# Optimization experiments

Hardware: AMD Instinct MI355X
Metric: run time of the kernel (lower is better)

## Reference

```python
import jax, jax.numpy as jnp
import numpy as np

B, C, IMG, P = 8, 3, 384, 16
D, H, L, MLP, NCLS = 384, 6, 12, 1536, 1000
G = IMG // P
T = G * G + 1  # 577 tokens incl CLS
GAMMA, MIN_TOKENS, EPS = 0.1, 16, 1e-6
LN_EPS = 1e-5


def _ln(x, s, b):
    m = x.mean(-1, keepdims=True)
    v = ((x - m) ** 2).mean(-1, keepdims=True)
    return (x - m) / jnp.sqrt(v + LN_EPS) * s + b


def _attn_block(xn, qw, qb, pw, pb):
    Bt, Tt, Dd = xn.shape
    hd = Dd // H
    qkv = (xn @ qw + qb).reshape(Bt, Tt, 3, H, hd).transpose(2, 0, 3, 1, 4)
    q, k, v = qkv[0], qkv[1], qkv[2]
    attn = jax.nn.softmax(jnp.einsum('bhqd,bhkd->bhqk', q, k) * (hd ** -0.5), axis=-1)
    out = jnp.einsum('bhqk,bhkd->bhqd', attn, v).transpose(0, 2, 1, 3).reshape(Bt, Tt, Dd)
    return attn, v, out @ pw + pb


def _cls_sensitivity(attn):
    # normalized entropy of the CLS attention row, mean over heads -> [B]
    cls = attn[:, :, 0, :]
    ent = -(cls * jnp.log(cls + EPS)).sum(-1)
    return (ent / jnp.log(float(attn.shape[-1]))).mean(1)


def _jacobian_importance(attn, v):
    # d(CLS)/d(patch_j) approx: CLS attention to patch j weighted by ||v_j||, summed over heads
    vnorm = jnp.linalg.norm(v, axis=-1)                   # [B,H,T]
    raw = (attn[:, :, 0, 1:] * vnorm[:, :, 1:]).sum(1)    # [B,N]
    mass = raw.sum(-1)                                    # [B]
    return raw / (mass[:, None] + EPS), mass


def _keep_ratio(rho, mass, prev_mass):
    delta = jnp.abs(mass - prev_mass) / (prev_mass + EPS)
    return jnp.clip(1.0 - GAMMA * (rho.mean() + delta.mean()), 0.0, 1.0)


def _mlp(xm, w1, b1, w2, b2):
    return jax.nn.gelu(xm @ w1 + b1, approximate=False) @ w2 + b2


def setup_inputs():
    key = jax.random.key(0)
    ks = jax.random.split(key, 9)
    s = 0.02
    return {
        'x': jax.random.normal(ks[0], (B, C, IMG, IMG), jnp.float32),
        'patch_w': jax.random.normal(ks[1], (C * P * P, D), jnp.float32) * s,
        'patch_b': jnp.zeros((D,), jnp.float32),
        'cls_token': jax.random.normal(ks[2], (1, 1, D), jnp.float32) * s,
        'pos_embed': jax.random.normal(ks[3], (1, T, D), jnp.float32) * s,
        'ln1_s': jnp.ones((L, D), jnp.float32), 'ln1_b': jnp.zeros((L, D), jnp.float32),
        'qkv_w': jax.random.normal(ks[4], (L, D, 3 * D), jnp.float32) * s,
        'qkv_b': jnp.zeros((L, 3 * D), jnp.float32),
        'proj_w': jax.random.normal(ks[5], (L, D, D), jnp.float32) * s,
        'proj_b': jnp.zeros((L, D), jnp.float32),
        'ln2_s': jnp.ones((L, D), jnp.float32), 'ln2_b': jnp.zeros((L, D), jnp.float32),
        'fc1_w': jax.random.normal(ks[6], (L, D, MLP), jnp.float32) * s,
        'fc1_b': jnp.zeros((L, MLP), jnp.float32),
        'fc2_w': jax.random.normal(ks[7], (L, MLP, D), jnp.float32) * s,
        'fc2_b': jnp.zeros((L, D), jnp.float32),
        'norm_s': jnp.ones((D,), jnp.float32), 'norm_b': jnp.zeros((D,), jnp.float32),
        'head_w': jax.random.normal(ks[8], (D, NCLS), jnp.float32) * s,
        'head_b': jnp.zeros((NCLS,), jnp.float32),
    }


def reference(x, patch_w, patch_b, cls_token, pos_embed, ln1_s, ln1_b, qkv_w, qkv_b,
              proj_w, proj_b, ln2_s, ln2_b, fc1_w, fc1_b, fc2_w, fc2_b,
              norm_s, norm_b, head_w, head_b):
    # NOTE: runs eagerly (no jit) because per-layer token counts are data-dependent,
    # mirroring the torch module's CPU syncs for index selection.
    Bc = x.shape[0]
    # patch embed: stride==kernel conv as a reshape+GEMM
    patches = x.reshape(Bc, C, G, P, G, P).transpose(0, 2, 4, 1, 3, 5).reshape(Bc, G * G, C * P * P)
    tok = patches @ patch_w + patch_b
    xcur = jnp.concatenate([jnp.broadcast_to(cls_token, (Bc, 1, D)), tok], axis=1) + pos_embed
    N = xcur.shape[1] - 1
    prev_mass = None
    for l in range(L):
        xn = _ln(xcur, ln1_s[l], ln1_b[l])
        attn, v, ao = _attn_block(xn, qkv_w[l], qkv_b[l], proj_w[l], proj_b[l])
        xcur = xcur + ao
        xcur = xcur + _mlp(_ln(xcur, ln2_s[l], ln2_b[l]), fc1_w[l], fc1_b[l], fc2_w[l], fc2_b[l])
        if N <= MIN_TOKENS:
            continue
        rho = _cls_sensitivity(attn)
        importance, mass = _jacobian_importance(attn, v)
        if prev_mass is not None:
            kr = float(_keep_ratio(rho, mass, prev_mass))
            N_next = max(MIN_TOKENS, int(N * kr))
        else:
            N_next = N
        if N_next < N:
            scores = importance.mean(0)  # shared across batch, matches x[:, keep_idx]
            _, idx = jax.lax.top_k(scores, N_next)
            keep = jnp.concatenate([jnp.zeros((1,), idx.dtype), jnp.sort(idx) + 1])
            xcur = xcur[:, keep]
            N = N_next
        prev_mass = mass
    xf = _ln(xcur, norm_s, norm_b)
    return xf[:, 0] @ head_w + head_b
```

## Files before the change

### kernel.cpp

```cpp
#include <hip/hip_runtime.h>
#include <math.h>

#define NHEADS 6
#define DMODEL 384
#define TMAXT  577
#define NMAXT  576
#define BATCH  8
#define LAYERS 12

typedef __attribute__((ext_vector_type(8))) short bf16x8v;
typedef __attribute__((ext_vector_type(4))) float f32x4v;

#define XSZ      (8ull*577*384)
#define X0_OFF   0ull
#define X1_OFF   (X0_OFF + XSZ)
#define XN_OFF   (X1_OFF + XSZ)
#define QKV_OFF  (XN_OFF + XSZ)
#define QKV_SZ   (8ull*577*1152)
#define AO_OFF   (QKV_OFF + QKV_SZ)
#define HBELEM   (8ull*577*1536)
#define RAWH_OFF (AO_OFF + XSZ)
#define RAWH_SZ  (8ull*6*576)
#define ENT_OFF  (RAWH_OFF + RAWH_SZ)
#define PM_OFF   (ENT_OFF + 64)
#define XF_OFF   (PM_OFF + 64)
#define KEEP_OFF (XF_OFF + 8*384)
#define T_OFF    (KEEP_OFF + 640)
#define TN_OFF   (T_OFF + 16)
#define WSPL_OFF (TN_OFF + 16)

#define W_QKV   0ull
#define W_PROJ  884736ull
#define W_FC1   1179648ull
#define W_FC2   2359296ull
#define W_PATCH 3538944ull

__device__ inline unsigned short rne_bf16(float f) {
    unsigned int u = __float_as_uint(f);
    u += 0x7FFFu + ((u >> 16) & 1u);
    return (unsigned short)(u >> 16);
}
__device__ inline float bf16_to_f(unsigned short h) {
    return __uint_as_float(((unsigned int)h) << 16);
}
__device__ inline void split_bf16(float x, unsigned short& h, unsigned short& l) {
    h = rne_bf16(x);
    l = rne_bf16(x - bf16_to_f(h));
}

__global__ __launch_bounds__(128) void prologue_kernel(const float* __restrict__ cls_tok,
                                                       const float* __restrict__ pos,
                                                       float* __restrict__ x0,
                                                       int* __restrict__ dT0)
{
    int b = blockIdx.x;
    for (int d = threadIdx.x; d < 384; d += 128)
        x0[(size_t)b*577*384 + d] = cls_tok[d] + pos[d];
    if (b == 0 && threadIdx.x == 0) *dT0 = 577;
}

__global__ __launch_bounds__(256) void psplit_kernel(const float* __restrict__ W,
                                                     unsigned short* __restrict__ dst,
                                                     int K, int N)
{
    int ktiles = K >> 5, ntiles = N >> 5;
    int tid = blockIdx.x;
    if (tid >= ktiles * ntiles) return;
    int tk = tid % ktiles, tn = tid / ktiles;
    int k0 = tk << 5, n0 = tn << 5;
    __shared__ unsigned short Th[32][34];
    __shared__ unsigned short Tl[32][34];
    int t = threadIdx.x;
    {
        int row = t >> 3, c4 = (t & 7) << 2;
        float4 wv = *(const float4*)(W + (size_t)(k0 + row) * N + n0 + c4);
        unsigned short h, l;
        split_bf16(wv.x, h, l); Th[c4+0][row] = h; Tl[c4+0][row] = l;
        split_bf16(wv.y, h, l); Th[c4+1][row] = h; Tl[c4+1][row] = l;
        split_bf16(wv.z, h, l); Th[c4+2][row] = h; Tl[c4+2][row] = l;
        split_bf16(wv.w, h, l); Th[c4+3][row] = h; Tl[c4+3][row] = l;
    }
    __syncthreads();
    {
        int n = t >> 3, k4 = (t & 7) << 2;
        unsigned short* dh = dst + (size_t)(n0 + n) * K + k0 + k4;
        unsigned short* dl = dh + (size_t)K * N;
        *(ushort4*)dh = make_ushort4(Th[n][k4], Th[n][k4+1], Th[n][k4+2], Th[n][k4+3]);
        *(ushort4*)dl = make_ushort4(Tl[n][k4], Tl[n][k4+1], Tl[n][k4+2], Tl[n][k4+3]);
    }
}

__global__ __launch_bounds__(256) void wsplit_kernel(const float* __restrict__ qkvw,
                                                     const float* __restrict__ projw,
                                                     const float* __restrict__ fc1w,
                                                     const float* __restrict__ fc2w,
                                                     unsigned short* __restrict__ wspl)
{
    int mat = blockIdx.y;
    const float* W; int K, N; size_t off;
    if (mat == 0)      { W = qkvw; K = 384;  N = 1152; off = W_QKV; }
    else if (mat == 1) { W = projw; K = 384; N = 384;  off = W_PROJ; }
    else if (mat == 2) { W = fc1w; K = 384;  N = 1536; off = W_FC1; }
    else               { W = fc2w; K = 1536; N = 384;  off = W_FC2; }
    int ktiles = K >> 5, ntiles = N >> 5;
    int tid = blockIdx.x;
    if (tid >= ktiles * ntiles) return;
    int tk = tid % ktiles, tn = tid / ktiles;
    int k0 = tk << 5, n0 = tn << 5;
    __shared__ unsigned short Th[32][34];
    __shared__ unsigned short Tl[32][34];
    int t = threadIdx.x;
    {
        int row = t >> 3, c4 = (t & 7) << 2;
        float4 wv = *(const float4*)(W + (size_t)(k0 + row) * N + n0 + c4);
        unsigned short h, l;
        split_bf16(wv.x, h, l); Th[c4+0][row] = h; Tl[c4+0][row] = l;
        split_bf16(wv.y, h, l); Th[c4+1][row] = h; Tl[c4+1][row] = l;
        split_bf16(wv.z, h, l); Th[c4+2][row] = h; Tl[c4+2][row] = l;
        split_bf16(wv.w, h, l); Th[c4+3][row] = h; Tl[c4+3][row] = l;
    }
    __syncthreads();
    {
        int n = t >> 3, k4 = (t & 7) << 2;
        unsigned short* dh = wspl + off + (size_t)(n0 + n) * K + k0 + k4;
        unsigned short* dl = dh + (size_t)K * N;
        *(ushort4*)dh = make_ushort4(Th[n][k4], Th[n][k4+1], Th[n][k4+2], Th[n][k4+3]);
        *(ushort4*)dl = make_ushort4(Tl[n][k4], Tl[n][k4+1], Tl[n][k4+2], Tl[n][k4+3]);
    }
}

__global__ __launch_bounds__(256, 4) void patch_mfma_kernel(const float* __restrict__ x,
                                                            const unsigned short* __restrict__ Wt,
                                                            const float* __restrict__ pb,
                                                            const float* __restrict__ pos,
                                                            float* __restrict__ x0)
{
    const int K = 768, N = 384, M = 4608;
    int m0 = blockIdx.y * 64;
    int n0 = blockIdx.x * 64;

    __shared__ unsigned short As[2][64][40];
    __shared__ unsigned short Bs[2][64][40];

    int t = threadIdx.x;
    int lane = t & 63, w = t >> 6;
    int wr = w >> 1, wc = w & 1;
    int quad = lane >> 4, l16 = lane & 15;

    f32x4v acc[2][2];
#pragma unroll
    for (int i = 0; i < 2; i++)
#pragma unroll
        for (int j = 0; j < 2; j++) acc[i][j] = (f32x4v){0.f, 0.f, 0.f, 0.f};

    int arow = t >> 2, ak8 = (t & 3) * 8;
    int garow = m0 + arow;
    int ab = garow / 576, att = garow % 576;
    int g1 = att / 24, g2 = att % 24;
    const float* xr = x + ((size_t)(ab*3)*384 + g1*16)*384 + g2*16;

    int bn = t >> 2, bk8 = (t & 3) * 8;
    const unsigned short* Bh = Wt + (size_t)(n0 + bn) * K + bk8;
    const unsigned short* Bl = Bh + (size_t)K * N;

    for (int k0 = 0; k0 < K; k0 += 32) {
        int k = k0 + ak8;
        int c = k >> 8, rr = k & 255, p1 = rr >> 4, p2 = rr & 15;
        const float* src = xr + ((size_t)c*384 + p1)*384 + p2;
        float4 f0 = *(const float4*)(src);
        float4 f1 = *(const float4*)(src + 4);
        float f[8] = {f0.x, f0.y, f0.z, f0.w, f1.x, f1.y, f1.z, f1.w};
        unsigned short ah[8], al[8];
#pragma unroll
        for (int j = 0; j < 8; j++) split_bf16(f[j], ah[j], al[j]);
        uint4 vbh = *(const uint4*)(Bh + k0);
        uint4 vbl = *(const uint4*)(Bl + k0);
        __syncthreads();
        *(uint4*)&As[0][arow][ak8] = *(uint4*)ah;
        *(uint4*)&As[1][arow][ak8] = *(uint4*)al;
        *(uint4*)&Bs[0][bn][bk8] = vbh;
        *(uint4*)&Bs[1][bn][bk8] = vbl;
        __syncthreads();

        bf16x8v afh[2], afl[2], bfh[2], bfl[2];
#pragma unroll
        for (int rb = 0; rb < 2; rb++) {
            int r = wr * 32 + rb * 16 + l16;
            afh[rb] = *(const bf16x8v*)&As[0][r][quad * 8];
            afl[rb] = *(const bf16x8v*)&As[1][r][quad * 8];
        }
#pragma unroll
        for (int cb = 0; cb < 2; cb++) {
            int cc = wc * 32 + cb * 16 + l16;
            bfh[cb] = *(const bf16x8v*)&Bs[0][cc][quad * 8];
            bfl[cb] = *(const bf16x8v*)&Bs[1][cc][quad * 8];
        }
#pragma unroll
        for (int rb = 0; rb < 2; rb++)
#pragma unroll
            for (int cb = 0; cb < 2; cb++) {
                acc[rb][cb] = __builtin_amdgcn_mfma_f32_16x16x32_bf16(afl[rb], bfh[cb], acc[rb][cb], 0, 0, 0);
                acc[rb][cb] = __builtin_amdgcn_mfma_f32_16x16x32_bf16(afh[rb], bfl[cb], acc[rb][cb], 0, 0, 0);
                acc[rb][cb] = __builtin_amdgcn_mfma_f32_16x16x32_bf16(afh[rb], bfh[cb], acc[rb][cb], 0, 0, 0);
            }
    }

#pragma unroll
    for (int rb = 0; rb < 2; rb++) {
#pragma unroll
        for (int reg = 0; reg < 4; reg++) {
            int r = m0 + wr * 32 + rb * 16 + quad * 4 + reg;
            if (r >= M) continue;
            int bb = r / 576, ttt = r % 576;
#pragma unroll
            for (int cb = 0; cb < 2; cb++) {
                int cc = n0 + wc * 32 + cb * 16 + l16;
                float v = acc[rb][cb][reg] + pb[cc] + pos[(size_t)(1 + ttt)*384 + cc];
                x0[(size_t)(bb*577 + 1 + ttt)*384 + cc] = v;
            }
        }
    }
}

__global__ __launch_bounds__(256) void ln_kernel(const float* __restrict__ xin,
                                                 const float* __restrict__ sc,
                                                 const float* __restrict__ bi,
                                                 unsigned short* __restrict__ yhi,
                                                 unsigned short* __restrict__ ylo,
                                                 const int* __restrict__ dT)
{
    int T = *dT;
    int M = 8 * T;
    int r = blockIdx.x * 4 + (threadIdx.x >> 6);
    if (r >= M) return;
    int lane = threadIdx.x & 63;
    const float* xr = xin + (size_t)r * 384;
    float v[6];
#pragma unroll
    for (int i = 0; i < 6; i++) v[i] = xr[lane + 64*i];
    float s = v[0]+v[1]+v[2]+v[3]+v[4]+v[5];
#pragma unroll
    for (int off = 32; off; off >>= 1) s += __shfl_xor(s, off, 64);
    float mean = s * (1.0f/384.0f);
    float q = 0.f;
#pragma unroll
    for (int i = 0; i < 6; i++) { float d = v[i]-mean; q += d*d; }
#pragma unroll
    for (int off = 32; off; off >>= 1) q += __shfl_xor(q, off, 64);
    float rstd = 1.0f / sqrtf(q * (1.0f/384.0f) + 1e-5f);
#pragma unroll
    for (int i = 0; i < 6; i++) {
        int d = lane + 64*i;
        float y = (v[i]-mean) * rstd * sc[d] + bi[d];
        unsigned short h, l;
        split_bf16(y, h, l);
        yhi[(size_t)r*384 + d] = h;
        ylo[(size_t)r*384 + d] = l;
    }
}

template<bool GELU>
__global__ __launch_bounds__(256, 3) void gemm3_kernel(const unsigned short* __restrict__ Ahi,
                                                       const unsigned short* __restrict__ Alo,
                                                       const unsigned short* __restrict__ Wt,
                                                       const float* __restrict__ bias,
                                                       unsigned short* __restrict__ Chi,
                                                       unsigned short* __restrict__ Clo,
                                                       int K, int N,
                                                       const int* __restrict__ dT)
{
    int T = *dT; int M = 8 * T;
    int m0 = blockIdx.y * 64;
    if (m0 >= M) return;
    int n0 = blockIdx.x * 128;

    __shared__ unsigned short As[2][64][40];
    __shared__ unsigned short Bs[2][128][40];

    int t = threadIdx.x;
    int lane = t & 63, w = t >> 6;
    int wr = w >> 1, wc = w & 1;
    int quad = lane >> 4, l16 = lane & 15;

    f32x4v acc[2][4];
#pragma unroll
    for (int i = 0; i < 2; i++)
#pragma unroll
        for (int j = 0; j < 4; j++) acc[i][j] = (f32x4v){0.f, 0.f, 0.f, 0.f};

    int arow = t >> 2, ak = (t & 3) * 8;
    int ag = m0 + arow; if (ag > M - 1) ag = M - 1;
    const unsigned short* Ah = Ahi + (size_t)ag * K + ak;
    const unsigned short* Al = Alo + (size_t)ag * K + ak;

    int bn = t >> 1, bk = (t & 1) * 16;
    const unsigned short* Bh = Wt + (size_t)(n0 + bn) * K + bk;
    const unsigned short* Bl = Bh + (size_t)K * N;

    for (int k0 = 0; k0 < K; k0 += 32) {
        uint4 vah  = *(const uint4*)(Ah + k0);
        uint4 val  = *(const uint4*)(Al + k0);
        uint4 vbh0 = *(const uint4*)(Bh + k0);
        uint4 vbh1 = *(const uint4*)(Bh + k0 + 8);
        uint4 vbl0 = *(const uint4*)(Bl + k0);
        uint4 vbl1 = *(const uint4*)(Bl + k0 + 8);
        __syncthreads();
        *(uint4*)&As[0][arow][ak] = vah;
        *(uint4*)&As[1][arow][ak] = val;
        *(uint4*)&Bs[0][bn][bk]     = vbh0;
        *(uint4*)&Bs[0][bn][bk + 8] = vbh1;
        *(uint4*)&Bs[1][bn][bk]     = vbl0;
        *(uint4*)&Bs[1][bn][bk + 8] = vbl1;
        __syncthreads();

        bf16x8v afh[2], afl[2], bfh[4], bfl[4];
#pragma unroll
        for (int rb = 0; rb < 2; rb++) {
            int r = wr * 32 + rb * 16 + l16;
            afh[rb] = *(const bf16x8v*)&As[0][r][quad * 8];
            afl[rb] = *(const bf16x8v*)&As[1][r][quad * 8];
        }
#pragma unroll
        for (int cb = 0; cb < 4; cb++) {
            int c = wc * 64 + cb * 16 + l16;
            bfh[cb] = *(const bf16x8v*)&Bs[0][c][quad * 8];
            bfl[cb] = *(const bf16x8v*)&Bs[1][c][quad * 8];
        }
#pragma unroll
        for (int rb = 0; rb < 2; rb++)
#pragma unroll
            for (int cb = 0; cb < 4; cb++) {
                acc[rb][cb] = __builtin_amdgcn_mfma_f32_16x16x32_bf16(afl[rb], bfh[cb], acc[rb][cb], 0, 0, 0);
                acc[rb][cb] = __builtin_amdgcn_mfma_f32_16x16x32_bf16(afh[rb], bfl[cb], acc[rb][cb], 0, 0, 0);
                acc[rb][cb] = __builtin_amdgcn_mfma_f32_16x16x32_bf16(afh[rb], bfh[cb], acc[rb][cb], 0, 0, 0);
            }
    }

#pragma unroll
    for (int rb = 0; rb < 2; rb++) {
#pragma unroll
        for (int reg = 0; reg < 4; reg++) {
            int r = m0 + wr * 32 + rb * 16 + quad * 4 + reg;
            if (r >= M) continue;
#pragma unroll
            for (int cb = 0; cb < 4; cb++) {
                int c = n0 + wc * 64 + cb * 16 + l16;
                float v = acc[rb][cb][reg] + bias[c];
                if (GELU) v = 0.5f * v * (1.0f + erff(v * 0.70710678118654752440f));
                unsigned short h, l;
                split_bf16(v, h, l);
                Chi[(size_t)r * N + c] = h;
                Clo[(size_t)r * N + c] = l;
            }
        }
    }
}

__global__ __launch_bounds__(256, 4) void gemm64_kernel(const unsigned short* __restrict__ Ahi,
                                                        const unsigned short* __restrict__ Alo,
                                                        const unsigned short* __restrict__ Wt,
                                                        const float* __restrict__ bias,
                                                        const float* __restrict__ resid,
                                                        float* __restrict__ Cf,
                                                        int K, int N,
                                                        const int* __restrict__ dT)
{
    int T = *dT; int M = 8 * T;
    int m0 = blockIdx.y * 64;
    if (m0 >= M) return;
    int n0 = blockIdx.x * 64;

    __shared__ unsigned short As[2][64][40];
    __shared__ unsigned short Bs[2][64][40];

    int t = threadIdx.x;
    int lane = t & 63, w = t >> 6;
    int wr = w >> 1, wc = w & 1;
    int quad = lane >> 4, l16 = lane & 15;

    f32x4v acc[2][2];
#pragma unroll
    for (int i = 0; i < 2; i++)
#pragma unroll
        for (int j = 0; j < 2; j++) acc[i][j] = (f32x4v){0.f, 0.f, 0.f, 0.f};

    int arow = t >> 2, ak = (t & 3) * 8;
    int ag = m0 + arow; if (ag > M - 1) ag = M - 1;
    const unsigned short* Ah = Ahi + (size_t)ag * K + ak;
    const unsigned short* Al = Alo + (size_t)ag * K + ak;

    int bn = t >> 2, bk = (t & 3) * 8;
    const unsigned short* Bh = Wt + (size_t)(n0 + bn) * K + bk;
    const unsigned short* Bl = Bh + (size_t)K * N;

    for (int k0 = 0; k0 < K; k0 += 32) {
        uint4 vah = *(const uint4*)(Ah + k0);
        uint4 val = *(const uint4*)(Al + k0);
        uint4 vbh = *(const uint4*)(Bh + k0);
        uint4 vbl = *(const uint4*)(Bl + k0);
        __syncthreads();
        *(uint4*)&As[0][arow][ak] = vah;
        *(uint4*)&As[1][arow][ak] = val;
        *(uint4*)&Bs[0][bn][bk] = vbh;
        *(uint4*)&Bs[1][bn][bk] = vbl;
        __syncthreads();

        bf16x8v afh[2], afl[2], bfh[2], bfl[2];
#pragma unroll
        for (int rb = 0; rb < 2; rb++) {
            int r = wr * 32 + rb * 16 + l16;
            afh[rb] = *(const bf16x8v*)&As[0][r][quad * 8];
            afl[rb] = *(const bf16x8v*)&As[1][r][quad * 8];
        }
#pragma unroll
        for (int cb = 0; cb < 2; cb++) {
            int c = wc * 32 + cb * 16 + l16;
            bfh[cb] = *(const bf16x8v*)&Bs[0][c][quad * 8];
            bfl[cb] = *(const bf16x8v*)&Bs[1][c][quad * 8];
        }
#pragma unroll
        for (int rb = 0; rb < 2; rb++)
#pragma unroll
            for (int cb = 0; cb < 2; cb++) {
                acc[rb][cb] = __builtin_amdgcn_mfma_f32_16x16x32_bf16(afl[rb], bfh[cb], acc[rb][cb], 0, 0, 0);
                acc[rb][cb] = __builtin_amdgcn_mfma_f32_16x16x32_bf16(afh[rb], bfl[cb], acc[rb][cb], 0, 0, 0);
                acc[rb][cb] = __builtin_amdgcn_mfma_f32_16x16x32_bf16(afh[rb], bfh[cb], acc[rb][cb], 0, 0, 0);
            }
    }

#pragma unroll
    for (int rb = 0; rb < 2; rb++) {
#pragma unroll
        for (int reg = 0; reg < 4; reg++) {
            int r = m0 + wr * 32 + rb * 16 + quad * 4 + reg;
            if (r >= M) continue;
#pragma unroll
            for (int cb = 0; cb < 2; cb++) {
                int c = n0 + wc * 32 + cb * 16 + l16;
                float v = acc[rb][cb][reg] + bias[c] + resid[(size_t)r * N + c];
                Cf[(size_t)r * N + c] = v;
            }
        }
    }
}

__global__ __launch_bounds__(256, 3) void attn_kernel(const unsigned short* __restrict__ qh,
                                                      const unsigned short* __restrict__ ql,
                                                      unsigned short* __restrict__ out_hi,
                                                      unsigned short* __restrict__ out_lo,
                                                      const int* __restrict__ dT)
{
    int T = *dT;
    int q0 = blockIdx.x * 64;
    if (q0 >= T) return;
    int bh = blockIdx.y;
    int b = bh / NHEADS, h = bh % NHEADS;

    __shared__ unsigned short Ks[2][64][72];
    __shared__ unsigned short Vt[2][64][72];
    __shared__ float Ss[64][66];
    __shared__ float m_s[64], l_s[64], al_s[64];

    int t = threadIdx.x;
    int lane = t & 63, w = t >> 6;
    int l16 = lane & 15, quad = lane >> 4;

    const bf16x8v zf = (bf16x8v){0,0,0,0,0,0,0,0};
    bf16x8v qf[2][2];
    {
        int gq = q0 + w * 16 + l16;
        bool valid = gq < T;
        size_t base = (size_t)(b * T + (valid ? gq : 0)) * 1152 + h * 64;
#pragma unroll
        for (int ks = 0; ks < 2; ks++) {
            int off = ks * 32 + quad * 8;
            qf[ks][0] = valid ? *(const bf16x8v*)(qh + base + off) : zf;
            qf[ks][1] = valid ? *(const bf16x8v*)(ql + base + off) : zf;
        }
    }
    if (t < 64) { m_s[t] = -INFINITY; l_s[t] = 0.f; }

    f32x4v oacc[4];
#pragma unroll
    for (int cb = 0; cb < 4; cb++) oacc[cb] = (f32x4v){0.f, 0.f, 0.f, 0.f};

    int ntiles = (T + 63) >> 6;
    for (int kt = 0; kt < ntiles; kt++) {
        int kbase = kt * 64;
        __syncthreads();

        {
            int gk = kbase + lane;
            int sd0 = w * 16;
            bool valid = gk < T;
            size_t base = (size_t)(b * T + (valid ? gk : 0)) * 1152 + 384 + h * 64 + sd0;
            const uint4 z4 = make_uint4(0,0,0,0);
            uint4 kh0 = valid ? *(const uint4*)(qh + base)     : z4;
            uint4 kh1 = valid ? *(const uint4*)(qh + base + 8) : z4;
            uint4 kl0 = valid ? *(const uint4*)(ql + base)     : z4;
            uint4 kl1 = valid ? *(const uint4*)(ql + base + 8) : z4;
            *(uint4*)&Ks[0][lane][sd0]     = kh0;
            *(uint4*)&Ks[0][lane][sd0 + 8] = kh1;
            *(uint4*)&Ks[1][lane][sd0]     = kl0;
            *(uint4*)&Ks[1][lane][sd0 + 8] = kl1;
            uint4 vh0 = valid ? *(const uint4*)(qh + base + 384)     : z4;
            uint4 vh1 = valid ? *(const uint4*)(qh + base + 384 + 8) : z4;
            uint4 vl0 = valid ? *(const uint4*)(ql + base + 384)     : z4;
            uint4 vl1 = valid ? *(const uint4*)(ql + base + 384 + 8) : z4;
            unsigned short th[16], tl[16];
            *(uint4*)&th[0] = vh0; *(uint4*)&th[8] = vh1;
            *(uint4*)&tl[0] = vl0; *(uint4*)&tl[8] = vl1;
#pragma unroll
            for (int i = 0; i < 16; i++) {
                Vt[0][sd0 + i][lane] = th[i];
                Vt[1][sd0 + i][lane] = tl[i];
            }
        }
        __syncthreads();

#pragma unroll
        for (int cb = 0; cb < 4; cb++) {
            f32x4v sacc = (f32x4v){0.f, 0.f, 0.f, 0.f};
#pragma unroll
            for (int ks = 0; ks < 2; ks++) {
                bf16x8v bhi = *(const bf16x8v*)&Ks[0][cb*16 + l16][ks*32 + quad*8];
                bf16x8v blo = *(const bf16x8v*)&Ks[1][cb*16 + l16][ks*32 + quad*8];
                sacc = __builtin_amdgcn_mfma_f32_16x16x32_bf16(qf[ks][1], bhi, sacc, 0, 0, 0);
                sacc = __builtin_amdgcn_mfma_f32_16x16x32_bf16(qf[ks][0], blo, sacc, 0, 0, 0);
                sacc = __builtin_amdgcn_mfma_f32_16x16x32_bf16(qf[ks][0], bhi, sacc, 0, 0, 0);
            }
            int col = cb*16 + l16;
            int gk = kbase + col;
#pragma unroll
            for (int reg = 0; reg < 4; reg++)
                Ss[w*16 + quad*4 + reg][col] = (gk < T) ? sacc[reg]*0.125f : -INFINITY;
        }
        __syncthreads();

        {
            int rr = t >> 2, sub = t & 3;
            float mx = -INFINITY;
#pragma unroll
            for (int kk = 0; kk < 16; kk++) mx = fmaxf(mx, Ss[rr][sub*16 + kk]);
            mx = fmaxf(mx, __shfl_xor(mx, 1, 64));
            mx = fmaxf(mx, __shfl_xor(mx, 2, 64));
            float mold = m_s[rr];
            float newm = fmaxf(mold, mx);
            float ps = 0.f;
#pragma unroll
            for (int kk = 0; kk < 16; kk++) {
                float p = __expf(Ss[rr][sub*16 + kk] - newm);
                unsigned short hh, ll;
                split_bf16(p, hh, ll);
                Ks[0][rr][sub*16 + kk] = hh;
                Ks[1][rr][sub*16 + kk] = ll;
                ps += p;
            }
            ps += __shfl_xor(ps, 1, 64);
            ps += __shfl_xor(ps, 2, 64);
            if (sub == 0) {
                float alpha = __expf(mold - newm);
                l_s[rr] = l_s[rr]*alpha + ps;
                m_s[rr] = newm;
                al_s[rr] = alpha;
            }
        }
        __syncthreads();

#pragma unroll
        for (int reg = 0; reg < 4; reg++) {
            float a = al_s[w*16 + quad*4 + reg];
#pragma unroll
            for (int cb = 0; cb < 4; cb++) oacc[cb][reg] *= a;
        }
#pragma unroll
        for (int ks = 0; ks < 2; ks++) {
            bf16x8v phi = *(const bf16x8v*)&Ks[0][w*16 + l16][ks*32 + quad*8];
            bf16x8v plo = *(const bf16x8v*)&Ks[1][w*16 + l16][ks*32 + quad*8];
#pragma unroll
            for (int cb = 0; cb < 4; cb++) {
                bf16x8v vhi = *(const bf16x8v*)&Vt[0][cb*16 + l16][ks*32 + quad*8];
                bf16x8v vlo = *(const bf16x8v*)&Vt[1][cb*16 + l16][ks*32 + quad*8];
                oacc[cb] = __builtin_amdgcn_mfma_f32_16x16x32_bf16(plo, vhi, oacc[cb], 0, 0, 0);
                oacc[cb] = __builtin_amdgcn_mfma_f32_16x16x32_bf16(phi, vlo, oacc[cb], 0, 0, 0);
                oacc[cb] = __builtin_amdgcn_mfma_f32_16x16x32_bf16(phi, vhi, oacc[cb], 0, 0, 0);
            }
        }
    }

#pragma unroll
    for (int reg = 0; reg < 4; reg++) {
        int gq = q0 + w*16 + quad*4 + reg;
        if (gq < T) {
            float inv = 1.0f / l_s[w*16 + quad*4 + reg];
#pragma unroll
            for (int cb = 0; cb < 4; cb++) {
                float v = oacc[cb][reg] * inv;
                unsigned short hh, ll;
                split_bf16(v, hh, ll);
                size_t o = (size_t)(b*T + gq)*384 + h*64 + cb*16 + l16;
                out_hi[o] = hh;
                out_lo[o] = ll;
            }
        }
    }
}

__global__ __launch_bounds__(256) void cls_stats_kernel(const unsigned short* __restrict__ qh,
                                                        const unsigned short* __restrict__ ql,
                                                        float* __restrict__ raw_h,
                                                        float* __restrict__ ent,
                                                        const int* __restrict__ dT)
{
    int T = *dT;
    int bh = blockIdx.x;
    int b = bh / NHEADS, h = bh % NHEADS;
    __shared__ float q0s[64];
    __shared__ float logit[TMAXT];
    __shared__ float red[8];
    int t = threadIdx.x;
    if (t < 64) {
        size_t o = (size_t)(b*T)*1152 + h*64 + t;
        q0s[t] = bf16_to_f(qh[o]) + bf16_to_f(ql[o]);
    }
    __syncthreads();
    float lmax = -INFINITY;
    for (int j = t; j < T; j += 256) {
        size_t o = (size_t)(b*T + j)*1152 + 384 + h*64;
        float dot = 0.f;
#pragma unroll
        for (int d = 0; d < 64; d += 4) {
            ushort4 a = *(const ushort4*)(qh + o + d);
            ushort4 c = *(const ushort4*)(ql + o + d);
            dot += q0s[d+0]*(bf16_to_f(a.x)+bf16_to_f(c.x));
            dot += q0s[d+1]*(bf16_to_f(a.y)+bf16_to_f(c.y));
            dot += q0s[d+2]*(bf16_to_f(a.z)+bf16_to_f(c.z));
            dot += q0s[d+3]*(bf16_to_f(a.w)+bf16_to_f(c.w));
        }
        float lg = dot * 0.125f;
        logit[j] = lg;
        lmax = fmaxf(lmax, lg);
    }
#pragma unroll
    for (int off = 32; off; off >>= 1) lmax = fmaxf(lmax, __shfl_xor(lmax, off, 64));
    if ((t & 63) == 0) red[t >> 6] = lmax;
    __syncthreads();
    float gmax = fmaxf(fmaxf(red[0], red[1]), fmaxf(red[2], red[3]));
    __syncthreads();
    float psum = 0.f;
    for (int j = t; j < T; j += 256) psum += expf(logit[j] - gmax);
#pragma unroll
    for (int off = 32; off; off >>= 1) psum += __shfl_xor(psum, off, 64);
    if ((t & 63) == 0) red[4 + (t >> 6)] = psum;
    __syncthreads();
    float inv = 1.0f / (red[4] + red[5] + red[6] + red[7]);
    float entp = 0.f;
    for (int j = t; j < T; j += 256) {
        float p = expf(logit[j] - gmax) * inv;
        entp += -p * logf(p + 1e-6f);
        if (j >= 1) {
            size_t o = (size_t)(b*T + j)*1152 + 768 + h*64;
            float vn = 0.f;
#pragma unroll
            for (int d = 0; d < 64; d += 4) {
                ushort4 a = *(const ushort4*)(qh + o + d);
                ushort4 c = *(const ushort4*)(ql + o + d);
                float v0 = bf16_to_f(a.x)+bf16_to_f(c.x);
                float v1 = bf16_to_f(a.y)+bf16_to_f(c.y);
                float v2 = bf16_to_f(a.z)+bf16_to_f(c.z);
                float v3 = bf16_to_f(a.w)+bf16_to_f(c.w);
                vn += v0*v0 + v1*v1 + v2*v2 + v3*v3;
            }
            raw_h[(size_t)bh*576 + (j - 1)] = p * sqrtf(vn);
        }
    }
#pragma unroll
    for (int off = 32; off; off >>= 1) entp += __shfl_xor(entp, off, 64);
    __syncthreads();
    if ((t & 63) == 0) red[t >> 6] = entp;
    __syncthreads();
    if (t == 0) ent[bh] = red[0] + red[1] + red[2] + red[3];
}

__global__ __launch_bounds__(256) void decide_kernel(const float* __restrict__ raw_h,
                                                     const float* __restrict__ ent,
                                                     float* __restrict__ prev_mass,
                                                     int* __restrict__ keep,
                                                     const int* __restrict__ dT,
                                                     int* __restrict__ dTnext,
                                                     int layer)
{
    int t = threadIdx.x;
    int T = *dT, N = T - 1;
    __shared__ float rbS[8][580];
    __shared__ float massS[8];
    __shared__ float pmS[8];
    __shared__ float esumS;
    __shared__ float scores[NMAXT];
    __shared__ int   keptFlag[NMAXT];
    __shared__ int   nnS;
    __shared__ int   wsum[4], wpre[4];

    if (N <= 16) {
        for (int i = t; i < T; i += 256) keep[i] = i;
        if (t == 0) *dTnext = T;
        return;
    }
    if (t < 8) pmS[t] = prev_mass[t];

    {
        int b = t >> 5, lane = t & 31;
        const float* base = raw_h + (size_t)b * 6 * 576;
        float s = 0.f;
        for (int j = lane; j < N; j += 32) {
            float a0 = base[0*576 + j];
            float a1 = base[1*576 + j];
            float a2 = base[2*576 + j];
            float a3 = base[3*576 + j];
            float a4 = base[4*576 + j];
            float a5 = base[5*576 + j];
            float rb = ((a0 + a1) + (a2 + a3)) + (a4 + a5);
            rbS[b][j] = rb;
            s += rb;
        }
#pragma unroll
        for (int off = 16; off; off >>= 1) s += __shfl_xor(s, off, 64);
        if (lane == 0) massS[b] = s;
    }
    if (t < 64) {
        float e = (t < 48) ? ent[t] : 0.f;
#pragma unroll
        for (int off = 32; off; off >>= 1) e += __shfl_xor(e, off, 64);
        if (t == 0) esumS = e;
    }
    __syncthreads();

    for (int j = t; j < N; j += 256) {
        float s = 0.f;
#pragma unroll
        for (int b = 0; b < 8; b++)
            s += rbS[b][j] / (massS[b] + 1e-6f);
        scores[j] = s * 0.125f;
    }
    __syncthreads();

    if (t == 0) {
        float rho_mean = esumS / 48.0f / logf((float)T);
        int Nn;
        if (layer == 0) {
            Nn = N;
        } else {
            float dm = 0.f;
#pragma unroll
            for (int b = 0; b < 8; b++)
                dm += fabsf(massS[b] - pmS[b]) / (pmS[b] + 1e-6f);
            dm *= 0.125f;
            float kr = 1.0f - 0.1f * (rho_mean + dm);
            kr = fminf(fmaxf(kr, 0.0f), 1.0f);
            Nn = (int)((double)N * (double)kr);
            if (Nn < 16) Nn = 16;
        }
        nnS = Nn;
        *dTnext = Nn + 1;
    }
    __syncthreads();
    if (t < 8) prev_mass[t] = massS[t];
    int Nn = nnS;

    if (Nn < N) {
        for (int j = t; j < N; j += 256) {
            float sj = scores[j];
            int cnt = 0;
            int j2 = 0;
            for (; j2 + 8 <= N; j2 += 8) {
                float x0 = scores[j2+0], x1 = scores[j2+1];
                float x2 = scores[j2+2], x3 = scores[j2+3];
                float x4 = scores[j2+4], x5 = scores[j2+5];
                float x6 = scores[j2+6], x7 = scores[j2+7];
                cnt += (x0 > sj) || (x0 == sj && j2+0 < j);
                cnt += (x1 > sj) || (x1 == sj && j2+1 < j);
                cnt += (x2 > sj) || (x2 == sj && j2+2 < j);
                cnt += (x3 > sj) || (x3 == sj && j2+3 < j);
                cnt += (x4 > sj) || (x4 == sj && j2+4 < j);
                cnt += (x5 > sj) || (x5 == sj && j2+5 < j);
                cnt += (x6 > sj) || (x6 == sj && j2+6 < j);
                cnt += (x7 > sj) || (x7 == sj && j2+7 < j);
            }
            for (; j2 < N; j2++) {
                float s2 = scores[j2];
                cnt += (s2 > sj) || (s2 == sj && j2 < j);
            }
            keptFlag[j] = (cnt < Nn) ? 1 : 0;
        }
        __syncthreads();

        int local = 0;
        int kf[3];
#pragma unroll
        for (int c = 0; c < 3; c++) {
            int j = 3*t + c;
            kf[c] = (j < N) ? keptFlag[j] : 0;
            local += kf[c];
        }
        int lane64 = t & 63, wv = t >> 6;
        int inc = local;
#pragma unroll
        for (int off = 1; off < 64; off <<= 1) {
            int nb = __shfl_up(inc, off, 64);
            if (lane64 >= off) inc += nb;
        }
        if (lane64 == 63) wsum[wv] = inc;
        __syncthreads();
        if (t == 0) {
            int run = 0;
#pragma unroll
            for (int i = 0; i < 4; i++) { wpre[i] = run; run += wsum[i]; }
            keep[0] = 0;
        }
        __syncthreads();
        int pos = 1 + (inc - local) + wpre[wv];
#pragma unroll
        for (int c = 0; c < 3; c++) {
            int j = 3*t + c;
            if (j < N && kf[c]) keep[pos++] = j + 1;
        }
    } else {
        for (int i = t; i < T; i += 256) keep[i] = i;
    }
}

__global__ __launch_bounds__(128) void gather_kernel(const float* __restrict__ src,
                                                     float* __restrict__ dst,
                                                     const int* __restrict__ keep,
                                                     const int* __restrict__ dT,
                                                     const int* __restrict__ dTnext)
{
    int Tn = *dTnext;
    int ti = blockIdx.x;
    if (ti >= Tn) return;
    int To = *dT;
    int b = blockIdx.y;
    const float* s = src + (size_t)(b*To + keep[ti]) * 384;
    float* d = dst + (size_t)(b*Tn + ti) * 384;
    int t = threadIdx.x;
    if (t < 96) ((float4*)d)[t] = ((const float4*)s)[t];
}

__global__ __launch_bounds__(64) void lnf_kernel(const float* __restrict__ xin,
                                                 const float* __restrict__ sc,
                                                 const float* __restrict__ bi,
                                                 float* __restrict__ xf,
                                                 const int* __restrict__ dT)
{
    int T = *dT;
    int b = blockIdx.x;
    int lane = threadIdx.x;
    const float* xr = xin + (size_t)(b*T) * 384;
    float v[6];
#pragma unroll
    for (int i = 0; i < 6; i++) v[i] = xr[lane + 64*i];
    float s = v[0]+v[1]+v[2]+v[3]+v[4]+v[5];
#pragma unroll
    for (int off = 32; off; off >>= 1) s += __shfl_xor(s, off, 64);
    float mean = s * (1.0f/384.0f);
    float q = 0.f;
#pragma unroll
    for (int i = 0; i < 6; i++) { float d = v[i]-mean; q += d*d; }
#pragma unroll
    for (int off = 32; off; off >>= 1) q += __shfl_xor(q, off, 64);
    float rstd = 1.0f / sqrtf(q * (1.0f/384.0f) + 1e-5f);
#pragma unroll
    for (int i = 0; i < 6; i++) {
        int d = lane + 64*i;
        xf[(size_t)b*384 + d] = (v[i]-mean) * rstd * sc[d] + bi[d];
    }
}

__global__ __launch_bounds__(256) void head_kernel(const float* __restrict__ xf,
                                                   const float* __restrict__ hw,
                                                   const float* __restrict__ hb,
                                                   float* __restrict__ out)
{
    int idx = blockIdx.x * 256 + threadIdx.x;
    if (idx >= 8000) return;
    int b = idx / 1000, n = idx - b*1000;
    const float* xr = xf + (size_t)b*384;
    float s = hb[n];
#pragma unroll 4
    for (int k = 0; k < 384; k++) s += xr[k] * hw[(size_t)k*1000 + n];
    out[idx] = s;
}

extern "C" void kernel_launch(void* const* d_in, const int* in_sizes, int n_in,
                              void* d_out, int out_size, void* d_ws, size_t ws_size,
                              hipStream_t stream)
{
    (void)in_sizes; (void)n_in; (void)out_size; (void)ws_size;
    const float* x       = (const float*)d_in[0];
    const float* patch_w = (const float*)d_in[1];
    const float* patch_b = (const float*)d_in[2];
    const float* cls_tok = (const float*)d_in[3];
    const float* pos     = (const float*)d_in[4];
    const float* ln1_s   = (const float*)d_in[5];
    const float* ln1_b   = (const float*)d_in[6];
    const float* qkv_w   = (const float*)d_in[7];
    const float* qkv_b   = (const float*)d_in[8];
    const float* proj_w  = (const float*)d_in[9];
    const float* proj_b  = (const float*)d_in[10];
    const float* ln2_s   = (const float*)d_in[11];
    const float* ln2_b   = (const float*)d_in[12];
    const float* fc1_w   = (const float*)d_in[13];
    const float* fc1_b   = (const float*)d_in[14];
    const float* fc2_w   = (const float*)d_in[15];
    const float* fc2_b   = (const float*)d_in[16];
    const float* norm_s  = (const float*)d_in[17];
    const float* norm_b  = (const float*)d_in[18];
    const float* head_w  = (const float*)d_in[19];
    const float* head_b  = (const float*)d_in[20];
    float* out = (float*)d_out;
    float* ws  = (float*)d_ws;

    float* x0   = ws + X0_OFF;
    float* x1   = ws + X1_OFF;
    float* rawh = ws + RAWH_OFF;
    float* entb = ws + ENT_OFF;
    float* pm   = ws + PM_OFF;
    float* xf   = ws + XF_OFF;
    int*   keep = (int*)(ws + KEEP_OFF);
    int*   dT0  = (int*)(ws + T_OFF);
    int*   dT1  = (int*)(ws + TN_OFF);

    unsigned short* xn_hi  = (unsigned short*)(ws + XN_OFF);
    unsigned short* xn_lo  = xn_hi + XSZ;
    unsigned short* qkv_hi = (unsigned short*)(ws + QKV_OFF);
    unsigned short* qkv_lo = qkv_hi + QKV_SZ;
    unsigned short* ao_hi  = (unsigned short*)(ws + AO_OFF);
    unsigned short* ao_lo  = ao_hi + XSZ;
    unsigned short* hb_hi  = (unsigned short*)(ws + QKV_OFF);
    unsigned short* hb_lo  = hb_hi + HBELEM;
    unsigned short* wspl   = (unsigned short*)(ws + WSPL_OFF);

    prologue_kernel<<<8, 128, 0, stream>>>(cls_tok, pos, x0, dT0);
    psplit_kernel<<<288, 256, 0, stream>>>(patch_w, wspl + W_PATCH, 768, 384);
    patch_mfma_kernel<<<dim3(6, 72), 256, 0, stream>>>(x, wspl + W_PATCH, patch_b, pos, x0);

    float* bufs[2] = { x0, x1 };
    for (int l = 0; l < LAYERS; l++) {
        float* src = bufs[l & 1];
        float* dst = bufs[(l + 1) & 1];
        int* cur = (l & 1) ? dT1 : dT0;
        int* nxt = (l & 1) ? dT0 : dT1;
        wsplit_kernel<<<dim3(576, 4), 256, 0, stream>>>(
            qkv_w + (size_t)l*384*1152, proj_w + (size_t)l*384*384,
            fc1_w + (size_t)l*384*1536, fc2_w + (size_t)l*1536*384, wspl);
        ln_kernel<<<1154, 256, 0, stream>>>(src, ln1_s + l*384, ln1_b + l*384, xn_hi, xn_lo, cur);
        gemm3_kernel<false><<<dim3(9, 73), 256, 0, stream>>>(
            xn_hi, xn_lo, wspl + W_QKV, qkv_b + l*1152, qkv_hi, qkv_lo, 384, 1152, cur);
        attn_kernel<<<dim3(10, 48), 256, 0, stream>>>(qkv_hi, qkv_lo, ao_hi, ao_lo, cur);
        cls_stats_kernel<<<48, 256, 0, stream>>>(qkv_hi, qkv_lo, rawh, entb, cur);
        gemm64_kernel<<<dim3(6, 73), 256, 0, stream>>>(
            ao_hi, ao_lo, wspl + W_PROJ, proj_b + l*384, src, src, 384, 384, cur);
        ln_kernel<<<1154, 256, 0, stream>>>(src, ln2_s + l*384, ln2_b + l*384, xn_hi, xn_lo, cur);
        gemm3_kernel<true><<<dim3(12, 73), 256, 0, stream>>>(
            xn_hi, xn_lo, wspl + W_FC1, fc1_b + l*1536, hb_hi, hb_lo, 384, 1536, cur);
        gemm64_kernel<<<dim3(6, 73), 256, 0, stream>>>(
            hb_hi, hb_lo, wspl + W_FC2, fc2_b + l*384, src, src, 1536, 384, cur);
        decide_kernel<<<1, 256, 0, stream>>>(rawh, entb, pm, keep, cur, nxt, l);
        gather_kernel<<<dim3(577, 8), 128, 0, stream>>>(src, dst, keep, cur, nxt);
    }
    lnf_kernel<<<8, 64, 0, stream>>>(bufs[0], norm_s, norm_b, xf, dT0);
    head_kernel<<<32, 256, 0, stream>>>(xf, head_w, head_b, out);
}
```

Before: 2.446 ms.

## Split single-block token-pruning decision into mass, rank, and finalize kernels

The single-block decide kernel is replaced by three kernels. The first computes per-batch mass and the entropy sum across 9 blocks. The second ranks token scores across 3 blocks, one token per thread, and writes keep flags to global memory. The third recomputes the keep count and does the prefix-sum compaction. This spreads the O(N^2) rank computation over more compute units, at the cost of two extra launches per layer and global round-trips for the intermediate values.

```diff
diff --git a/kernel.cpp b/kernel.cpp
--- a/kernel.cpp
+++ b/kernel.cpp
@@ -35,6 +35,10 @@
 #define W_FC2   2359296ull
 #define W_PATCH 3538944ull
 
+#define MASS_OFF  (WSPL_OFF + 2064384)
+#define ESUM_OFF  (MASS_OFF + 16)
+#define KFLAG_OFF (ESUM_OFF + 16)
+
 __device__ inline unsigned short rne_bf16(float f) {
     unsigned int u = __float_as_uint(f);
     u += 0x7FFFu + ((u >> 16) & 1u);
@@ -46,6 +50,25 @@
 __device__ inline void split_bf16(float x, unsigned short& h, unsigned short& l) {
     h = rne_bf16(x);
     l = rne_bf16(x - bf16_to_f(h));
+}
+
+__device__ inline int compute_Nn(const float* __restrict__ massG,
+                                 const float* __restrict__ pm,
+                                 const float* __restrict__ esumG,
+                                 int N, int T, int layer)
+{
+    if (layer == 0) return N;
+    float rho_mean = (*esumG) / 48.0f / logf((float)T);
+    float dm = 0.f;
+#pragma unroll
+    for (int b = 0; b < 8; b++)
+        dm += fabsf(massG[b] - pm[b]) / (pm[b] + 1e-6f);
+    dm *= 0.125f;
+    float kr = 1.0f - 0.1f * (rho_mean + dm);
+    kr = fminf(fmaxf(kr, 0.0f), 1.0f);
+    int Nn = (int)((double)N * (double)kr);
+    if (Nn < 16) Nn = 16;
+    return Nn;
 }
 
 __global__ __launch_bounds__(128) void prologue_kernel(const float* __restrict__ cls_tok,
@@ -682,37 +705,64 @@
     if (t == 0) ent[bh] = red[0] + red[1] + red[2] + red[3];
 }
 
-__global__ __launch_bounds__(256) void decide_kernel(const float* __restrict__ raw_h,
-                                                     const float* __restrict__ ent,
-                                                     float* __restrict__ prev_mass,
-                                                     int* __restrict__ keep,
-                                                     const int* __restrict__ dT,
-                                                     int* __restrict__ dTnext,
-                                                     int layer)
-{
+__global__ __launch_bounds__(256) void dmass_kernel(const float* __restrict__ raw_h,
+                                                    const float* __restrict__ ent,
+                                                    float* __restrict__ massG,
+                                                    float* __restrict__ esumG,
+                                                    const int* __restrict__ dT)
+{
+    int T = *dT, N = T - 1;
+    if (N <= 16) return;
+    int b = blockIdx.x;
     int t = threadIdx.x;
+    if (b == 8) {
+        if (t < 64) {
+            float e = (t < 48) ? ent[t] : 0.f;
+#pragma unroll
+            for (int off = 32; off; off >>= 1) e += __shfl_xor(e, off, 64);
+            if (t == 0) *esumG = e;
+        }
+        return;
+    }
+    __shared__ float red[4];
+    const float* base = raw_h + (size_t)b * 6 * 576;
+    float s = 0.f;
+    for (int j = t; j < N; j += 256) {
+        float a0 = base[0*576 + j];
+        float a1 = base[1*576 + j];
+        float a2 = base[2*576 + j];
+        float a3 = base[3*576 + j];
+        float a4 = base[4*576 + j];
+        float a5 = base[5*576 + j];
+        s += ((a0 + a1) + (a2 + a3)) + (a4 + a5);
+    }
+#pragma unroll
+    for (int off = 32; off; off >>= 1) s += __shfl_xor(s, off, 64);
+    if ((t & 63) == 0) red[t >> 6] = s;
+    __syncthreads();
+    if (t == 0) massG[b] = red[0] + red[1] + red[2] + red[3];
+}
+
+__global__ __launch_bounds__(256) void drank_kernel(const float* __restrict__ raw_h,
+                                                    const float* __restrict__ massG,
+                                                    const float* __restrict__ pm,
+                                                    const float* __restrict__ esumG,
+                                                    int* __restrict__ keptFlagG,
+                                                    const int* __restrict__ dT,
+                                                    int layer)
+{
     int T = *dT, N = T - 1;
-    __shared__ float rbS[8][580];
-    __shared__ float massS[8];
-    __shared__ float pmS[8];
-    __shared__ float esumS;
+    if (N <= 16 || layer == 0) return;
+    int Nn = compute_Nn(massG, pm, esumG, N, T, layer);
+    if (Nn >= N) return;
+
     __shared__ float scores[NMAXT];
-    __shared__ int   keptFlag[NMAXT];
-    __shared__ int   nnS;
-    __shared__ int   wsum[4], wpre[4];
-
-    if (N <= 16) {
-        for (int i = t; i < T; i += 256) keep[i] = i;
-        if (t == 0) *dTnext = T;
-        return;
-    }
-    if (t < 8) pmS[t] = prev_mass[t];
-
-    {
-        int b = t >> 5, lane = t & 31;
-        const float* base = raw_h + (size_t)b * 6 * 576;
+    int t = threadIdx.x;
+    for (int j = t; j < N; j += 256) {
         float s = 0.f;
-        for (int j = lane; j < N; j += 32) {
+#pragma unroll
+        for (int b = 0; b < 8; b++) {
+            const float* base = raw_h + (size_t)b * 6 * 576;
             float a0 = base[0*576 + j];
             float a1 = base[1*576 + j];
             float a2 = base[2*576 + j];
@@ -720,86 +770,72 @@
             float a4 = base[4*576 + j];
             float a5 = base[5*576 + j];
             float rb = ((a0 + a1) + (a2 + a3)) + (a4 + a5);
-            rbS[b][j] = rb;
-            s += rb;
-        }
-#pragma unroll
-        for (int off = 16; off; off >>= 1) s += __shfl_xor(s, off, 64);
-        if (lane == 0) massS[b] = s;
-    }
-    if (t < 64) {
-        float e = (t < 48) ? ent[t] : 0.f;
-#pragma unroll
-        for (int off = 32; off; off >>= 1) e += __shfl_xor(e, off, 64);
-        if (t == 0) esumS = e;
+            s += rb / (massG[b] + 1e-6f);
+        }
+        scores[j] = s * 0.125f;
     }
     __syncthreads();
 
-    for (int j = t; j < N; j += 256) {
-        float s = 0.f;
-#pragma unroll
-        for (int b = 0; b < 8; b++)
-            s += rbS[b][j] / (massS[b] + 1e-6f);
-        scores[j] = s * 0.125f;
-    }
-    __syncthreads();
-
+    int j = blockIdx.x * 256 + t;
+    if (j >= N) return;
+    float sj = scores[j];
+    int cnt = 0;
+    int j2 = 0;
+    for (; j2 + 8 <= N; j2 += 8) {
+        float x0 = scores[j2+0], x1 = scores[j2+1];
+        float x2 = scores[j2+2], x3 = scores[j2+3];
+        float x4 = scores[j2+4], x5 = scores[j2+5];
+        float x6 = scores[j2+6], x7 = scores[j2+7];
+        cnt += (x0 > sj) || (x0 == sj && j2+0 < j);
+        cnt += (x1 > sj) || (x1 == sj && j2+1 < j);
+        cnt += (x2 > sj) || (x2 == sj && j2+2 < j);
+        cnt += (x3 > sj) || (x3 == sj && j2+3 < j);
+        cnt += (x4 > sj) || (x4 == sj && j2+4 < j);
+        cnt += (x5 > sj) || (x5 == sj && j2+5 < j);
+        cnt += (x6 > sj) || (x6 == sj && j2+6 < j);
+        cnt += (x7 > sj) || (x7 == sj && j2+7 < j);
+    }
+    for (; j2 < N; j2++) {
+        float s2 = scores[j2];
+        cnt += (s2 > sj) || (s2 == sj && j2 < j);
+    }
+    keptFlagG[j] = (cnt < Nn) ? 1 : 0;
+}
+
+__global__ __launch_bounds__(256) void dfin_kernel(const float* __restrict__ massG,
+                                                   const float* __restrict__ esumG,
+                                                   float* __restrict__ pm,
+                                                   const int* __restrict__ keptFlagG,
+                                                   int* __restrict__ keep,
+                                                   const int* __restrict__ dT,
+                                                   int* __restrict__ dTnext,
+                                                   int layer)
+{
+    int t = threadIdx.x;
+    int T = *dT, N = T - 1;
+    if (N <= 16) {
+        for (int i = t; i < T; i += 256) keep[i] = i;
+        if (t == 0) *dTnext = T;
+        return;
+    }
+    __shared__ int nnS;
+    __shared__ int wsum[4], wpre[4];
     if (t == 0) {
-        float rho_mean = esumS / 48.0f / logf((float)T);
-        int Nn;
-        if (layer == 0) {
-            Nn = N;
-        } else {
-            float dm = 0.f;
-#pragma unroll
-            for (int b = 0; b < 8; b++)
-                dm += fabsf(massS[b] - pmS[b]) / (pmS[b] + 1e-6f);
-            dm *= 0.125f;
-            float kr = 1.0f - 0.1f * (rho_mean + dm);
-            kr = fminf(fmaxf(kr, 0.0f), 1.0f);
-            Nn = (int)((double)N * (double)kr);
-            if (Nn < 16) Nn = 16;
-        }
+        int Nn = compute_Nn(massG, pm, esumG, N, T, layer);
         nnS = Nn;
         *dTnext = Nn + 1;
     }
     __syncthreads();
-    if (t < 8) prev_mass[t] = massS[t];
+    if (t < 8) pm[t] = massG[t];
     int Nn = nnS;
 
     if (Nn < N) {
-        for (int j = t; j < N; j += 256) {
-            float sj = scores[j];
-            int cnt = 0;
-            int j2 = 0;
-            for (; j2 + 8 <= N; j2 += 8) {
-                float x0 = scores[j2+0], x1 = scores[j2+1];
-                float x2 = scores[j2+2], x3 = scores[j2+3];
-                float x4 = scores[j2+4], x5 = scores[j2+5];
-                float x6 = scores[j2+6], x7 = scores[j2+7];
-                cnt += (x0 > sj) || (x0 == sj && j2+0 < j);
-                cnt += (x1 > sj) || (x1 == sj && j2+1 < j);
-                cnt += (x2 > sj) || (x2 == sj && j2+2 < j);
-                cnt += (x3 > sj) || (x3 == sj && j2+3 < j);
-                cnt += (x4 > sj) || (x4 == sj && j2+4 < j);
-                cnt += (x5 > sj) || (x5 == sj && j2+5 < j);
-                cnt += (x6 > sj) || (x6 == sj && j2+6 < j);
-                cnt += (x7 > sj) || (x7 == sj && j2+7 < j);
-            }
-            for (; j2 < N; j2++) {
-                float s2 = scores[j2];
-                cnt += (s2 > sj) || (s2 == sj && j2 < j);
-            }
-            keptFlag[j] = (cnt < Nn) ? 1 : 0;
-        }
-        __syncthreads();
-
         int local = 0;
         int kf[3];
 #pragma unroll
         for (int c = 0; c < 3; c++) {
             int j = 3*t + c;
-            kf[c] = (j < N) ? keptFlag[j] : 0;
+            kf[c] = (j < N) ? keptFlagG[j] : 0;
             local += kf[c];
         }
         int lane64 = t & 63, wv = t >> 6;
@@ -920,15 +956,18 @@
     float* out = (float*)d_out;
     float* ws  = (float*)d_ws;
 
-    float* x0   = ws + X0_OFF;
-    float* x1   = ws + X1_OFF;
-    float* rawh = ws + RAWH_OFF;
-    float* entb = ws + ENT_OFF;
-    float* pm   = ws + PM_OFF;
-    float* xf   = ws + XF_OFF;
-    int*   keep = (int*)(ws + KEEP_OFF);
-    int*   dT0  = (int*)(ws + T_OFF);
-    int*   dT1  = (int*)(ws + TN_OFF);
+    float* x0    = ws + X0_OFF;
+    float* x1    = ws + X1_OFF;
+    float* rawh  = ws + RAWH_OFF;
+    float* entb  = ws + ENT_OFF;
+    float* pm    = ws + PM_OFF;
+    float* xf    = ws + XF_OFF;
+    float* massG = ws + MASS_OFF;
+    float* esumG = ws + ESUM_OFF;
+    int*   kflag = (int*)(ws + KFLAG_OFF);
+    int*   keep  = (int*)(ws + KEEP_OFF);
+    int*   dT0   = (int*)(ws + T_OFF);
+    int*   dT1   = (int*)(ws + TN_OFF);
 
     unsigned short* xn_hi  = (unsigned short*)(ws + XN_OFF);
     unsigned short* xn_lo  = xn_hi + XSZ;
@@ -965,7 +1004,9 @@
             xn_hi, xn_lo, wspl + W_FC1, fc1_b + l*1536, hb_hi, hb_lo, 384, 1536, cur);
         gemm64_kernel<<<dim3(6, 73), 256, 0, stream>>>(
             hb_hi, hb_lo, wspl + W_FC2, fc2_b + l*384, src, src, 1536, 384, cur);
-        decide_kernel<<<1, 256, 0, stream>>>(rawh, entb, pm, keep, cur, nxt, l);
+        dmass_kernel<<<9, 256, 0, stream>>>(rawh, entb, massG, esumG, cur);
+        drank_kernel<<<3, 256, 0, stream>>>(rawh, massG, pm, esumG, kflag, cur, l);
+        dfin_kernel<<<1, 256, 0, stream>>>(massG, esumG, pm, kflag, keep, cur, nxt, l);
         gather_kernel<<<dim3(577, 8), 128, 0, stream>>>(src, dst, keep, cur, nxt);
     }
     lnf_kernel<<<8, 64, 0, stream>>>(bufs[0], norm_s, norm_b, xf, dT0);
```

New measurement: 2.345 ms. 1.04x faster.
